# Kernel optimization log

Measured on AMD Instinct MI355X. Metric: run time of the kernel, lower is better.

The kernel has to match this reference:

```python
import jax, jax.numpy as jnp
import numpy as np

D_MODEL = 1024
N_HEADS = 8
D_KEYS = D_MODEL // N_HEADS  # 128
D_LLM = 4096


def setup_inputs() -> dict:
    key = jax.random.key(0)
    ks = jax.random.split(key, 11)
    Bm, Lq, Vs = 8, 1024, 2048
    inner = D_KEYS * N_HEADS  # 1024
    s = 0.02
    return {
        "Q": jax.random.normal(ks[0], (Bm, Lq, D_MODEL), jnp.float32),
        "K_src": jax.random.normal(ks[1], (Vs, D_LLM), jnp.float32),
        "V_src": jax.random.normal(ks[2], (Vs, D_LLM), jnp.float32),
        "Wq": jax.random.normal(ks[3], (D_MODEL, inner), jnp.float32) * s,
        "bq": jnp.zeros((inner,), jnp.float32),
        "Wk": jax.random.normal(ks[4], (D_LLM, inner), jnp.float32) * s,
        "bk": jnp.zeros((inner,), jnp.float32),
        "Wv": jax.random.normal(ks[5], (D_LLM, inner), jnp.float32) * s,
        "bv": jnp.zeros((inner,), jnp.float32),
        "Wo": jax.random.normal(ks[6], (inner, D_LLM), jnp.float32) * s,
        "bo": jnp.zeros((D_LLM,), jnp.float32),
    }


def reference(Q, K_src, V_src, Wq, bq, Wk, bk, Wv, bv, Wo, bo):
    Bm, Lq, _ = Q.shape
    Vs, d_llm = K_src.shape
    H = N_HEADS
    Ek = d_llm // H  # NOTE: torch code scales by d_llm//H, not d_keys
    q = (Q @ Wq + bq).reshape(Bm, Lq, H, -1)           # [B,Lq,H,E]
    k = (K_src @ Wk + bk).reshape(Vs, H, -1)            # [S,H,E]
    v = (V_src @ Wv + bv).reshape(Vs, H, -1)            # [S,H,E]
    scale = 1.0 / jnp.sqrt(jnp.asarray(Ek, q.dtype))
    scores = jnp.einsum("blhe,she->bhls", q, k)         # [B,H,Lq,S]
    A = jax.nn.softmax(scale * scores, axis=-1)         # dropout = identity (eval)
    out = jnp.einsum("bhls,she->blhe", A, v)            # [B,Lq,H,E]
    out = out.reshape(Bm, Lq, -1)
    return out @ Wo + bo                                 # [B,Lq,d_llm]
```

## Files before the change

kernel.cpp:

```cpp
#include <hip/hip_runtime.h>
#include <hip/hip_bf16.h>


typedef __bf16 bf16x8 __attribute__((ext_vector_type(8)));
typedef float  f32x4  __attribute__((ext_vector_type(4)));

union V16 { uint4 u; bf16x8 v; };
__device__ __forceinline__ bf16x8 ld16v(const void* p) {
  V16 t; t.u = *(const uint4*)p; return t.v;
}
__device__ __forceinline__ uint4 pack8(float4 a, float4 b) {
  V16 t;
  t.v[0] = (__bf16)a.x; t.v[1] = (__bf16)a.y; t.v[2] = (__bf16)a.z; t.v[3] = (__bf16)a.w;
  t.v[4] = (__bf16)b.x; t.v[5] = (__bf16)b.y; t.v[6] = (__bf16)b.z; t.v[7] = (__bf16)b.w;
  return t.u;
}
__device__ __forceinline__ void dma16(const void* g, void* l) {
  __builtin_amdgcn_global_load_lds(
      (const __attribute__((address_space(1))) unsigned int*)g,
      (__attribute__((address_space(3))) unsigned int*)l, 16, 0, 0);
}
__device__ __forceinline__ float exp2_fast(float x) {
  float r;
  asm("v_exp_f32 %0, %1\n\ts_nop 1" : "=v"(r) : "v"(x));
  return r;
}
__device__ __forceinline__ int chunk_of(int row, int gc) {
  return row * 4 + (gc ^ ((row >> 1) & 3));
}

__global__ __launch_bounds__(256) void transpose_k(const float* __restrict__ W,
                                                   __bf16* __restrict__ Wt, int K, int N,
                                                   float scale) {
  __shared__ __bf16 t[32][33];
  int tx = threadIdx.x & 31, ty = threadIdx.x >> 5;
  int n0 = blockIdx.x * 32, k0 = blockIdx.y * 32;
#pragma unroll
  for (int r = 0; r < 32; r += 8)
    t[ty + r][tx] = (__bf16)(W[(size_t)(k0 + ty + r) * N + n0 + tx] * scale);
  __syncthreads();
#pragma unroll
  for (int r = 0; r < 32; r += 8) Wt[(size_t)(n0 + ty + r) * K + k0 + tx] = t[tx][ty + r];
}

template <typename AT, typename CT>
__device__ __forceinline__ void gemm_core(__bf16* As, __bf16* Bs,
                                          const AT* __restrict__ A,
                                          const __bf16* __restrict__ Bt,
                                          const float* __restrict__ bias,
                                          CT* __restrict__ C,
                                          int M, int N, int K, int lda, int ldb, int trans,
                                          int m0, int n0, float bscale) {
  const int tid = threadIdx.x;
  const int lane = tid & 63, wave = tid >> 6;
  const int g = lane >> 4, l16 = lane & 15;
  const int wr = wave >> 1, wc = wave & 1;
  int aoff[4], boff[4];
#pragma unroll
  for (int mf = 0; mf < 4; mf++) aoff[mf] = chunk_of(wr * 64 + mf * 16 + l16, g) * 8;
#pragma unroll
  for (int nf = 0; nf < 4; nf++) boff[nf] = chunk_of(wc * 64 + nf * 16 + l16, g) * 8;

  f32x4 acc[4][4] = {};
  for (int k0 = 0; k0 < K; k0 += 32) {
    __syncthreads();
    if constexpr (sizeof(AT) == 2) {
#pragma unroll
      for (int rnd = 0; rnd < 2; rnd++) {
        int cstart = wave * 128 + rnd * 64;
        int p = cstart + lane;
        int row = p >> 2, gc = (p & 3) ^ ((row >> 1) & 3);
        dma16((const __bf16*)A + (size_t)(m0 + row) * lda + k0 + gc * 8,
              As + (size_t)cstart * 8);
      }
    } else {
#pragma unroll
      for (int i = 0; i < 2; i++) {
        int p = tid + i * 256;
        int row = p >> 2, gc = (p & 3) ^ ((row >> 1) & 3);
        const float* ap = (const float*)A + (size_t)(m0 + row) * lda + k0 + gc * 8;
        float4 f0 = *(const float4*)ap;
        float4 f1 = *(const float4*)(ap + 4);
        *(uint4*)(As + p * 8) = pack8(f0, f1);
      }
    }
#pragma unroll
    for (int rnd = 0; rnd < 2; rnd++) {
      int cstart = wave * 128 + rnd * 64;
      int p = cstart + lane;
      int row = p >> 2, gc = (p & 3) ^ ((row >> 1) & 3);
      dma16(Bt + (size_t)(n0 + row) * (size_t)ldb + k0 + gc * 8,
            Bs + (size_t)cstart * 8);
    }
    __syncthreads();
    bf16x8 af[4], bff[4];
#pragma unroll
    for (int mf = 0; mf < 4; mf++) af[mf]  = ld16v(As + aoff[mf]);
#pragma unroll
    for (int nf = 0; nf < 4; nf++) bff[nf] = ld16v(Bs + boff[nf]);
#pragma unroll
    for (int mf = 0; mf < 4; mf++)
#pragma unroll
      for (int nf = 0; nf < 4; nf++)
        acc[mf][nf] = __builtin_amdgcn_mfma_f32_16x16x32_bf16(af[mf], bff[nf], acc[mf][nf], 0, 0, 0);
  }
#pragma unroll
  for (int nf = 0; nf < 4; nf++) {
    int col = n0 + wc * 64 + nf * 16 + l16;
    float bv = bias[col] * bscale;
#pragma unroll
    for (int mf = 0; mf < 4; mf++) {
      int rowb = m0 + wr * 64 + mf * 16 + g * 4;
      if constexpr (sizeof(CT) == 2) {
        if (trans) {
          union { __bf16 h[4]; uint2 u; } pk;
#pragma unroll
          for (int r = 0; r < 4; r++) pk.h[r] = (__bf16)(acc[mf][nf][r] + bv);
          *(uint2*)&((__bf16*)C)[(size_t)col * M + rowb] = pk.u;
        } else {
#pragma unroll
          for (int r = 0; r < 4; r++)
            ((__bf16*)C)[(size_t)(rowb + r) * N + col] = (__bf16)(acc[mf][nf][r] + bv);
        }
      } else {
#pragma unroll
        for (int r = 0; r < 4; r++)
          ((float*)C)[(size_t)(rowb + r) * N + col] = acc[mf][nf][r] + bv;
      }
    }
  }
}

__global__ __launch_bounds__(256) void gemm_qkv(
    const float* __restrict__ Q,   const __bf16* __restrict__ WqT, const float* __restrict__ bq, __bf16* __restrict__ qb, float qscale,
    const float* __restrict__ Ksr, const __bf16* __restrict__ WkT, const float* __restrict__ bk, __bf16* __restrict__ kp0, __bf16* __restrict__ kp1,
    const float* __restrict__ Vsr, const __bf16* __restrict__ WvT, const float* __restrict__ bv, __bf16* __restrict__ vp0, __bf16* __restrict__ vp1) {
  __shared__ __align__(16) __bf16 As[128 * 32];
  __shared__ __align__(16) __bf16 Bs[128 * 32];
  const int bid = blockIdx.x;
  if (bid < 256) {
    const int m0 = (bid & 63) * 128, n0 = (bid >> 6) * 256;
    gemm_core<float, __bf16>(As, Bs, Q, WqT, bq, qb, 8192, 1024, 1024, 1024, 1024, 0,
                             m0, n0, qscale);
    gemm_core<float, __bf16>(As, Bs, Q, WqT, bq, qb, 8192, 1024, 1024, 1024, 1024, 0,
                             m0, n0 + 128, qscale);
  } else if (bid < 512) {
    const int b = bid - 256;
    const int grp = b >> 7, bb = b & 127;
    __bf16* dst = grp ? kp1 : kp0;
    gemm_core<float, __bf16>(As, Bs, Ksr + grp * 2048, WkT + grp * 2048, bk, dst,
                             2048, 1024, 2048, 4096, 4096, 0,
                             (bb & 15) * 128, (bb >> 4) * 128, grp == 0 ? 1.0f : 0.0f);
  } else {
    const int b = bid - 512;
    const int grp = b >> 7, bb = b & 127;
    __bf16* dst = grp ? vp1 : vp0;
    gemm_core<float, __bf16>(As, Bs, Vsr + grp * 2048, WvT + grp * 2048, bv, dst,
                             2048, 1024, 2048, 4096, 4096, 1,
                             (bb & 15) * 128, (bb >> 4) * 128, grp == 0 ? 1.0f : 0.0f);
  }
}

__global__ __launch_bounds__(256) void finalize2(
    const __bf16* __restrict__ kp0, const __bf16* __restrict__ kp1, __bf16* __restrict__ kb,
    const __bf16* __restrict__ vp0, const __bf16* __restrict__ vp1, __bf16* __restrict__ vtb) {
  int i = blockIdx.x * 256 + threadIdx.x;
  const __bf16 *a, *b;
  __bf16* d;
  int j;
  if (i < 262144) { a = kp0; b = kp1; d = kb;  j = i; }
  else            { a = vp0; b = vp1; d = vtb; j = i - 262144; }
  bf16x8 x = ld16v(a + (size_t)j * 8);
  bf16x8 y = ld16v(b + (size_t)j * 8);
  V16 o;
#pragma unroll
  for (int t = 0; t < 8; t++) o.v[t] = (__bf16)((float)x[t] + (float)y[t]);
  *(uint4*)(d + (size_t)j * 8) = o.u;
}

__global__ __launch_bounds__(256) void gemm_b_f(const __bf16* __restrict__ A,
                                                const __bf16* __restrict__ Bt,
                                                const float* __restrict__ bias,
                                                float* __restrict__ C,
                                                int M, int N, int K, int lda, int trans) {
  __shared__ __align__(16) __bf16 As[128 * 32];
  __shared__ __align__(16) __bf16 Bs[128 * 32];
  gemm_core<__bf16, float>(As, Bs, A, Bt, bias, C, M, N, K, lda, K, trans,
                           blockIdx.x * 128, blockIdx.y * 128, 1.0f);
}

__global__ __launch_bounds__(512, 4) void attn_k(const __bf16* q,
                                                 const __bf16* __restrict__ k,
                                                 const __bf16* __restrict__ vt,
                                                 __bf16* o) {
  __shared__ __align__(16) __bf16 ks[2][64 * 128];
  __shared__ __align__(16) __bf16 vs[2][128 * 64];
  __shared__ __align__(16) __bf16 ps[128 * 64];
  const int tid = threadIdx.x, lane = tid & 63, wave = tid >> 6;
  const int g = lane >> 4, l16 = lane & 15;
  const int h = blockIdx.y, q0 = blockIdx.x * 128;

  const __bf16* kbase = k + (size_t)h * 128;
  const __bf16* vbase = vt + (size_t)(h * 128) * 2048;

  bf16x8 qf[4];
#pragma unroll
  for (int kk = 0; kk < 4; kk++)
    qf[kk] = ld16v(q + (size_t)(q0 + wave * 16 + l16) * 1024 + h * 128 + kk * 32 + g * 8);

  f32x4 accO[8] = {};
  float m_i[4], l_i[4];
#pragma unroll
  for (int r = 0; r < 4; r++) { m_i[r] = -1e30f; l_i[r] = 0.f; }

  {
#pragma unroll
    for (int i = 0; i < 2; i++) {
      int c = wave * 128 + i * 64 + lane;
      int row = c >> 4, gc = (c & 15) ^ (row & 7);
      dma16(kbase + (size_t)row * 1024 + gc * 8, &ks[0][(wave * 128 + i * 64) * 8]);
    }
#pragma unroll
    for (int i = 0; i < 2; i++) {
      int c = wave * 128 + i * 64 + lane;
      int row = c >> 3, cc = (c & 7) ^ (row & 7);
      dma16(vbase + (size_t)row * 2048 + cc * 8, &vs[0][(wave * 128 + i * 64) * 8]);
    }
  }

  for (int t = 0; t < 32; t++) {
    const int cur = t & 1;
    asm volatile("s_waitcnt lgkmcnt(0)" ::: "memory");
    __builtin_amdgcn_s_barrier();
    __builtin_amdgcn_sched_barrier(0);
    {
      const int sn = ((t + 1) & 31) * 64;
#pragma unroll
      for (int i = 0; i < 2; i++) {
        int c = wave * 128 + i * 64 + lane;
        int row = c >> 4, gc = (c & 15) ^ (row & 7);
        dma16(kbase + (size_t)(sn + row) * 1024 + gc * 8,
              &ks[cur ^ 1][(wave * 128 + i * 64) * 8]);
      }
#pragma unroll
      for (int i = 0; i < 2; i++) {
        int c = wave * 128 + i * 64 + lane;
        int row = c >> 3, cc = (c & 7) ^ (row & 7);
        dma16(vbase + (size_t)row * 2048 + sn + cc * 8,
              &vs[cur ^ 1][(wave * 128 + i * 64) * 8]);
      }
    }
    asm volatile("s_waitcnt vmcnt(4)" ::: "memory");
    __builtin_amdgcn_s_barrier();
    __builtin_amdgcn_sched_barrier(0);

    f32x4 sc[4] = {};
    __builtin_amdgcn_s_setprio(1);
#pragma unroll
    for (int kk = 0; kk < 4; kk++) {
      bf16x8 kf[4];
#pragma unroll
      for (int nf = 0; nf < 4; nf++) {
        int row = nf * 16 + l16;
        kf[nf] = ld16v(&ks[cur][(row * 16 + ((kk * 4 + g) ^ (row & 7))) * 8]);
      }
#pragma unroll
      for (int nf = 0; nf < 4; nf++)
        sc[nf] = __builtin_amdgcn_mfma_f32_16x16x32_bf16(qf[kk], kf[nf], sc[nf], 0, 0, 0);
    }
    __builtin_amdgcn_s_setprio(0);

#pragma unroll
    for (int r = 0; r < 4; r++) {
      float mx = fmaxf(fmaxf(sc[0][r], sc[1][r]), fmaxf(sc[2][r], sc[3][r]));
#pragma unroll
      for (int off = 1; off < 16; off <<= 1) mx = fmaxf(mx, __shfl_xor(mx, off));
      float mn = fmaxf(m_i[r], mx);
      float alpha = exp2_fast(m_i[r] - mn);
      float rs = 0.f;
#pragma unroll
      for (int nf = 0; nf < 4; nf++) {
        float p = exp2_fast(sc[nf][r] - mn);
        sc[nf][r] = p;
        rs += p;
      }
#pragma unroll
      for (int off = 1; off < 16; off <<= 1) rs += __shfl_xor(rs, off);
      m_i[r] = mn;
      l_i[r] = l_i[r] * alpha + rs;
#pragma unroll
      for (int ef = 0; ef < 8; ef++) accO[ef][r] *= alpha;
    }

#pragma unroll
    for (int nf = 0; nf < 4; nf++)
#pragma unroll
      for (int r = 0; r < 4; r++) {
        int prow = wave * 16 + g * 4 + r;
        int cc = nf * 2 + (l16 >> 3);
        ps[(prow * 8 + (cc ^ (prow & 7))) * 8 + (l16 & 7)] = (__bf16)sc[nf][r];
      }

    __builtin_amdgcn_s_setprio(1);
#pragma unroll
    for (int kk = 0; kk < 2; kk++) {
      int prow = wave * 16 + l16;
      bf16x8 pf = ld16v(&ps[(prow * 8 + ((kk * 4 + g) ^ (prow & 7))) * 8]);
#pragma unroll
      for (int ef = 0; ef < 8; ef++) {
        int vrow = ef * 16 + l16;
        bf16x8 vf = ld16v(&vs[cur][(vrow * 8 + ((kk * 4 + g) ^ (vrow & 7))) * 8]);
        accO[ef] = __builtin_amdgcn_mfma_f32_16x16x32_bf16(pf, vf, accO[ef], 0, 0, 0);
      }
    }
    __builtin_amdgcn_s_setprio(0);
  }

  float inv[4];
#pragma unroll
  for (int r = 0; r < 4; r++) inv[r] = 1.0f / l_i[r];
#pragma unroll
  for (int ef = 0; ef < 8; ef++)
#pragma unroll
    for (int r = 0; r < 4; r++) {
      int row = q0 + wave * 16 + g * 4 + r;
      o[(size_t)row * 1024 + h * 128 + ef * 16 + l16] = (__bf16)(accO[ef][r] * inv[r]);
    }
}

extern "C" void kernel_launch(void* const* d_in, const int* in_sizes, int n_in,
                              void* d_out, int out_size, void* d_ws, size_t ws_size,
                              hipStream_t stream) {
  const float* Q   = (const float*)d_in[0];
  const float* Ksr = (const float*)d_in[1];
  const float* Vsr = (const float*)d_in[2];
  const float* Wq  = (const float*)d_in[3];
  const float* bq  = (const float*)d_in[4];
  const float* Wk  = (const float*)d_in[5];
  const float* bk  = (const float*)d_in[6];
  const float* Wv  = (const float*)d_in[7];
  const float* bv  = (const float*)d_in[8];
  const float* Wo  = (const float*)d_in[9];
  const float* bo  = (const float*)d_in[10];
  __bf16* ws = (__bf16*)d_ws;
  const size_t MB = 1024 * 1024;
  __bf16* qb  = ws;
  __bf16* kb  = ws + 8  * MB;
  __bf16* vtb = ws + 10 * MB;
  __bf16* kp0 = ws + 12 * MB;
  __bf16* kp1 = ws + 14 * MB;
  __bf16* vp0 = ws + 16 * MB;
  __bf16* vp1 = ws + 18 * MB;
  __bf16* WqT = ws + 20 * MB;
  __bf16* WkT = ws + 21 * MB;
  __bf16* WvT = ws + 25 * MB;
  __bf16* WoT = ws + 29 * MB;

  const float qscale = 0.044194173824159216f * 1.4426950408889634f;

  transpose_k<<<dim3(32, 32),  256, 0, stream>>>(Wq, WqT, 1024, 1024, qscale);
  transpose_k<<<dim3(32, 128), 256, 0, stream>>>(Wk, WkT, 4096, 1024, 1.0f);
  transpose_k<<<dim3(32, 128), 256, 0, stream>>>(Wv, WvT, 4096, 1024, 1.0f);
  transpose_k<<<dim3(128, 32), 256, 0, stream>>>(Wo, WoT, 1024, 4096, 1.0f);

  gemm_qkv<<<dim3(768), 256, 0, stream>>>(Q, WqT, bq, qb, qscale,
                                          Ksr, WkT, bk, kp0, kp1,
                                          Vsr, WvT, bv, vp0, vp1);
  finalize2<<<dim3(2048), 256, 0, stream>>>(kp0, kp1, kb, vp0, vp1, vtb);
  attn_k<<<dim3(64, 8), 512, 0, stream>>>(qb, kb, vtb, qb);
  gemm_b_f<<<dim3(64, 32), 256, 0, stream>>>(qb, WoT, bo, (float*)d_out, 8192, 4096, 1024, 1024, 0);
}
```

Measured before the change: 636.6 us.

## Software-pipeline the fp32-input QKV GEMM with register prefetch and double-buffered B

Splits the shared GEMM core into an fp32-A variant and a bf16-A variant. The fp32 variant used by the QKV projection keeps the next A tile in registers and double-buffers the B tile in LDS via async global_load_lds, waiting only on partial vmcnt, so global loads overlap the MFMA work. It also raises wave priority around the MFMA block. The intent is to hide load latency in the projection GEMMs at the cost of extra LDS and registers. The hand-written waitcnt counts could be wrong and break correctness.

```diff
diff --git a/kernel.cpp b/kernel.cpp
--- a/kernel.cpp
+++ b/kernel.cpp
@@ -43,14 +43,48 @@
   for (int r = 0; r < 32; r += 8) Wt[(size_t)(n0 + ty + r) * K + k0 + tx] = t[tx][ty + r];
 }
 
-template <typename AT, typename CT>
-__device__ __forceinline__ void gemm_core(__bf16* As, __bf16* Bs,
-                                          const AT* __restrict__ A,
-                                          const __bf16* __restrict__ Bt,
-                                          const float* __restrict__ bias,
-                                          CT* __restrict__ C,
-                                          int M, int N, int K, int lda, int ldb, int trans,
-                                          int m0, int n0, float bscale) {
+template <typename CT>
+__device__ __forceinline__ void gemm_epilogue(f32x4 (&acc)[4][4],
+                                              const float* __restrict__ bias,
+                                              CT* __restrict__ C,
+                                              int M, int N, int trans,
+                                              int m0, int n0, float bscale,
+                                              int wr, int wc, int g, int l16) {
+#pragma unroll
+  for (int nf = 0; nf < 4; nf++) {
+    int col = n0 + wc * 64 + nf * 16 + l16;
+    float bv = bias[col] * bscale;
+#pragma unroll
+    for (int mf = 0; mf < 4; mf++) {
+      int rowb = m0 + wr * 64 + mf * 16 + g * 4;
+      if constexpr (sizeof(CT) == 2) {
+        if (trans) {
+          union { __bf16 h[4]; uint2 u; } pk;
+#pragma unroll
+          for (int r = 0; r < 4; r++) pk.h[r] = (__bf16)(acc[mf][nf][r] + bv);
+          *(uint2*)&((__bf16*)C)[(size_t)col * M + rowb] = pk.u;
+        } else {
+#pragma unroll
+          for (int r = 0; r < 4; r++)
+            ((__bf16*)C)[(size_t)(rowb + r) * N + col] = (__bf16)(acc[mf][nf][r] + bv);
+        }
+      } else {
+#pragma unroll
+        for (int r = 0; r < 4; r++)
+          ((float*)C)[(size_t)(rowb + r) * N + col] = acc[mf][nf][r] + bv;
+      }
+    }
+  }
+}
+
+template <typename CT>
+__device__ __forceinline__ void gemm_core_f32(__bf16* As, __bf16* Bs0, __bf16* Bs1,
+                                              const float* __restrict__ A,
+                                              const __bf16* __restrict__ Bt,
+                                              const float* __restrict__ bias,
+                                              CT* __restrict__ C,
+                                              int M, int N, int K, int lda, int ldb, int trans,
+                                              int m0, int n0, float bscale) {
   const int tid = threadIdx.x;
   const int lane = tid & 63, wave = tid >> 6;
   const int g = lane >> 4, l16 = lane & 15;
@@ -61,36 +95,95 @@
 #pragma unroll
   for (int nf = 0; nf < 4; nf++) boff[nf] = chunk_of(wc * 64 + nf * 16 + l16, g) * 8;
 
+  const int p0 = tid, p1 = tid + 256;
+  const int ar0 = p0 >> 2, ag0 = (p0 & 3) ^ ((ar0 >> 1) & 3);
+  const int ar1 = p1 >> 2, ag1 = (p1 & 3) ^ ((ar1 >> 1) & 3);
+  const float* aptr0 = A + (size_t)(m0 + ar0) * lda + ag0 * 8;
+  const float* aptr1 = A + (size_t)(m0 + ar1) * lda + ag1 * 8;
+
+  f32x4 acc[4][4] = {};
+  float4 a0l, a0h, a1l, a1h;
+  a0l = *(const float4*)aptr0; a0h = *(const float4*)(aptr0 + 4);
+  a1l = *(const float4*)aptr1; a1h = *(const float4*)(aptr1 + 4);
+#pragma unroll
+  for (int rnd = 0; rnd < 2; rnd++) {
+    int c = wave * 128 + rnd * 64 + lane;
+    int row = c >> 2, gc = (c & 3) ^ ((row >> 1) & 3);
+    dma16(Bt + (size_t)(n0 + row) * (size_t)ldb + gc * 8,
+          Bs0 + (wave * 128 + rnd * 64) * 8);
+  }
+
+  const int T = K >> 5;
+  for (int t = 0; t < T; t++) {
+    __bf16* Bc = (t & 1) ? Bs1 : Bs0;
+    __bf16* Bn = (t & 1) ? Bs0 : Bs1;
+    const int kn = (t + 1 < T) ? (t + 1) * 32 : 0;
+    asm volatile("s_waitcnt lgkmcnt(0)" ::: "memory");
+    __builtin_amdgcn_s_barrier();
+    *(uint4*)(As + p0 * 8) = pack8(a0l, a0h);
+    *(uint4*)(As + p1 * 8) = pack8(a1l, a1h);
+    a0l = *(const float4*)(aptr0 + kn); a0h = *(const float4*)(aptr0 + kn + 4);
+    a1l = *(const float4*)(aptr1 + kn); a1h = *(const float4*)(aptr1 + kn + 4);
+#pragma unroll
+    for (int rnd = 0; rnd < 2; rnd++) {
+      int c = wave * 128 + rnd * 64 + lane;
+      int row = c >> 2, gc = (c & 3) ^ ((row >> 1) & 3);
+      dma16(Bt + (size_t)(n0 + row) * (size_t)ldb + kn + gc * 8,
+            Bn + (wave * 128 + rnd * 64) * 8);
+    }
+    asm volatile("s_waitcnt vmcnt(6) lgkmcnt(0)" ::: "memory");
+    __builtin_amdgcn_s_barrier();
+
+    bf16x8 af[4], bff[4];
+#pragma unroll
+    for (int mf = 0; mf < 4; mf++) af[mf]  = ld16v(As + aoff[mf]);
+#pragma unroll
+    for (int nf = 0; nf < 4; nf++) bff[nf] = ld16v(Bc + boff[nf]);
+    __builtin_amdgcn_s_setprio(1);
+#pragma unroll
+    for (int mf = 0; mf < 4; mf++)
+#pragma unroll
+      for (int nf = 0; nf < 4; nf++)
+        acc[mf][nf] = __builtin_amdgcn_mfma_f32_16x16x32_bf16(af[mf], bff[nf], acc[mf][nf], 0, 0, 0);
+    __builtin_amdgcn_s_setprio(0);
+  }
+  gemm_epilogue(acc, bias, C, M, N, trans, m0, n0, bscale, wr, wc, g, l16);
+}
+
+template <typename CT>
+__device__ __forceinline__ void gemm_core_b16(__bf16* As, __bf16* Bs,
+                                              const __bf16* __restrict__ A,
+                                              const __bf16* __restrict__ Bt,
+                                              const float* __restrict__ bias,
+                                              CT* __restrict__ C,
+                                              int M, int N, int K, int lda, int ldb, int trans,
+                                              int m0, int n0, float bscale) {
+  const int tid = threadIdx.x;
+  const int lane = tid & 63, wave = tid >> 6;
+  const int g = lane >> 4, l16 = lane & 15;
+  const int wr = wave >> 1, wc = wave & 1;
+  int aoff[4], boff[4];
+#pragma unroll
+  for (int mf = 0; mf < 4; mf++) aoff[mf] = chunk_of(wr * 64 + mf * 16 + l16, g) * 8;
+#pragma unroll
+  for (int nf = 0; nf < 4; nf++) boff[nf] = chunk_of(wc * 64 + nf * 16 + l16, g) * 8;
+
   f32x4 acc[4][4] = {};
   for (int k0 = 0; k0 < K; k0 += 32) {
     __syncthreads();
-    if constexpr (sizeof(AT) == 2) {
-#pragma unroll
-      for (int rnd = 0; rnd < 2; rnd++) {
-        int cstart = wave * 128 + rnd * 64;
-        int p = cstart + lane;
-        int row = p >> 2, gc = (p & 3) ^ ((row >> 1) & 3);
-        dma16((const __bf16*)A + (size_t)(m0 + row) * lda + k0 + gc * 8,
-              As + (size_t)cstart * 8);
-      }
-    } else {
-#pragma unroll
-      for (int i = 0; i < 2; i++) {
-        int p = tid + i * 256;
-        int row = p >> 2, gc = (p & 3) ^ ((row >> 1) & 3);
-        const float* ap = (const float*)A + (size_t)(m0 + row) * lda + k0 + gc * 8;
-        float4 f0 = *(const float4*)ap;
-        float4 f1 = *(const float4*)(ap + 4);
-        *(uint4*)(As + p * 8) = pack8(f0, f1);
-      }
-    }
 #pragma unroll
     for (int rnd = 0; rnd < 2; rnd++) {
       int cstart = wave * 128 + rnd * 64;
       int p = cstart + lane;
       int row = p >> 2, gc = (p & 3) ^ ((row >> 1) & 3);
-      dma16(Bt + (size_t)(n0 + row) * (size_t)ldb + k0 + gc * 8,
-            Bs + (size_t)cstart * 8);
+      dma16(A + (size_t)(m0 + row) * lda + k0 + gc * 8, As + (size_t)cstart * 8);
+    }
+#pragma unroll
+    for (int rnd = 0; rnd < 2; rnd++) {
+      int cstart = wave * 128 + rnd * 64;
+      int p = cstart + lane;
+      int row = p >> 2, gc = (p & 3) ^ ((row >> 1) & 3);
+      dma16(Bt + (size_t)(n0 + row) * (size_t)ldb + k0 + gc * 8, Bs + (size_t)cstart * 8);
     }
     __syncthreads();
     bf16x8 af[4], bff[4];
@@ -104,31 +197,7 @@
       for (int nf = 0; nf < 4; nf++)
         acc[mf][nf] = __builtin_amdgcn_mfma_f32_16x16x32_bf16(af[mf], bff[nf], acc[mf][nf], 0, 0, 0);
   }
-#pragma unroll
-  for (int nf = 0; nf < 4; nf++) {
-    int col = n0 + wc * 64 + nf * 16 + l16;
-    float bv = bias[col] * bscale;
-#pragma unroll
-    for (int mf = 0; mf < 4; mf++) {
-      int rowb = m0 + wr * 64 + mf * 16 + g * 4;
-      if constexpr (sizeof(CT) == 2) {
-        if (trans) {
-          union { __bf16 h[4]; uint2 u; } pk;
-#pragma unroll
-          for (int r = 0; r < 4; r++) pk.h[r] = (__bf16)(acc[mf][nf][r] + bv);
-          *(uint2*)&((__bf16*)C)[(size_t)col * M + rowb] = pk.u;
-        } else {
-#pragma unroll
-          for (int r = 0; r < 4; r++)
-            ((__bf16*)C)[(size_t)(rowb + r) * N + col] = (__bf16)(acc[mf][nf][r] + bv);
-        }
-      } else {
-#pragma unroll
-        for (int r = 0; r < 4; r++)
-          ((float*)C)[(size_t)(rowb + r) * N + col] = acc[mf][nf][r] + bv;
-      }
-    }
-  }
+  gemm_epilogue(acc, bias, C, M, N, trans, m0, n0, bscale, wr, wc, g, l16);
 }
 
 __global__ __launch_bounds__(256) void gemm_qkv(
@@ -136,28 +205,28 @@
     const float* __restrict__ Ksr, const __bf16* __restrict__ WkT, const float* __restrict__ bk, __bf16* __restrict__ kp0, __bf16* __restrict__ kp1,
     const float* __restrict__ Vsr, const __bf16* __restrict__ WvT, const float* __restrict__ bv, __bf16* __restrict__ vp0, __bf16* __restrict__ vp1) {
   __shared__ __align__(16) __bf16 As[128 * 32];
-  __shared__ __align__(16) __bf16 Bs[128 * 32];
+  __shared__ __align__(16) __bf16 Bs[2][128 * 32];
   const int bid = blockIdx.x;
   if (bid < 256) {
     const int m0 = (bid & 63) * 128, n0 = (bid >> 6) * 256;
-    gemm_core<float, __bf16>(As, Bs, Q, WqT, bq, qb, 8192, 1024, 1024, 1024, 1024, 0,
-                             m0, n0, qscale);
-    gemm_core<float, __bf16>(As, Bs, Q, WqT, bq, qb, 8192, 1024, 1024, 1024, 1024, 0,
-                             m0, n0 + 128, qscale);
+    gemm_core_f32<__bf16>(As, Bs[0], Bs[1], Q, WqT, bq, qb, 8192, 1024, 1024, 1024, 1024, 0,
+                          m0, n0, qscale);
+    gemm_core_f32<__bf16>(As, Bs[0], Bs[1], Q, WqT, bq, qb, 8192, 1024, 1024, 1024, 1024, 0,
+                          m0, n0 + 128, qscale);
   } else if (bid < 512) {
     const int b = bid - 256;
     const int grp = b >> 7, bb = b & 127;
     __bf16* dst = grp ? kp1 : kp0;
-    gemm_core<float, __bf16>(As, Bs, Ksr + grp * 2048, WkT + grp * 2048, bk, dst,
-                             2048, 1024, 2048, 4096, 4096, 0,
-                             (bb & 15) * 128, (bb >> 4) * 128, grp == 0 ? 1.0f : 0.0f);
+    gemm_core_f32<__bf16>(As, Bs[0], Bs[1], Ksr + grp * 2048, WkT + grp * 2048, bk, dst,
+                          2048, 1024, 2048, 4096, 4096, 0,
+                          (bb & 15) * 128, (bb >> 4) * 128, grp == 0 ? 1.0f : 0.0f);
   } else {
     const int b = bid - 512;
     const int grp = b >> 7, bb = b & 127;
     __bf16* dst = grp ? vp1 : vp0;
-    gemm_core<float, __bf16>(As, Bs, Vsr + grp * 2048, WvT + grp * 2048, bv, dst,
-                             2048, 1024, 2048, 4096, 4096, 1,
-                             (bb & 15) * 128, (bb >> 4) * 128, grp == 0 ? 1.0f : 0.0f);
+    gemm_core_f32<__bf16>(As, Bs[0], Bs[1], Vsr + grp * 2048, WvT + grp * 2048, bv, dst,
+                          2048, 1024, 2048, 4096, 4096, 1,
+                          (bb & 15) * 128, (bb >> 4) * 128, grp == 0 ? 1.0f : 0.0f);
   }
 }
 
@@ -185,8 +254,8 @@
                                                 int M, int N, int K, int lda, int trans) {
   __shared__ __align__(16) __bf16 As[128 * 32];
   __shared__ __align__(16) __bf16 Bs[128 * 32];
-  gemm_core<__bf16, float>(As, Bs, A, Bt, bias, C, M, N, K, lda, K, trans,
-                           blockIdx.x * 128, blockIdx.y * 128, 1.0f);
+  gemm_core_b16<float>(As, Bs, A, Bt, bias, C, M, N, K, lda, K, trans,
+                       blockIdx.x * 128, blockIdx.y * 128, 1.0f);
 }
 
 __global__ __launch_bounds__(512, 4) void attn_k(const __bf16* q,
```

After: 622.2 us. 1.02x faster.
